# Kernel optimization log

Hardware: AMD Instinct MI355X
Metric: run time of the kernel (lower is better)

The kernel has to match this reference:

```python
import jax, jax.numpy as jnp
import numpy as np

B, S, H = 4, 2048, 768
ROUTING_GAIN = 1.0
LN_EPS = 1e-5
MAS_EPS = 1e-9


def _mas_normalize(logits):
    m = jnp.max(jnp.abs(logits), axis=-1, keepdims=True)
    return jax.nn.relu(logits / (m + MAS_EPS))


def _layer_norm(x, w, b):
    mu = jnp.mean(x, axis=-1, keepdims=True)
    var = jnp.var(x, axis=-1, keepdims=True)
    return (x - mu) / jnp.sqrt(var + LN_EPS) * w + b


def _spl(x, proto, gate, mu_w, mu_b):
    # SparseProtoLinear: comp = x @ mu_w.T + mu_b ; match = x @ proto.T / sqrt(d_in) ; gate_logit = x @ gate.T
    scale = 1.0 / jnp.sqrt(jnp.asarray(x.shape[-1], x.dtype))
    match = jnp.einsum('bsd,od->bso', x, proto) * scale
    gate_logit = jnp.einsum('bsd,od->bso', x, gate)
    comp = jnp.einsum('bsd,od->bso', x, mu_w) + mu_b
    return comp, match, gate_logit


def _gate_branch(inp, comp, match, gate_logit):
    routing_logits = (match - _mas_normalize(gate_logit)) * ROUTING_GAIN
    return (inp + comp) * _mas_normalize(routing_logits)


def _rotate_half(x):
    x1, x2 = jnp.split(x, 2, axis=-1)
    return jnp.concatenate([-x2, x1], axis=-1)


def _apply_rope(q, k, cos, sin):
    return q * cos + _rotate_half(q) * sin, k * cos + _rotate_half(k) * sin


def _causal_attention(q, k, v):
    # single-head SDPA over full hidden dim, causal
    d = q.shape[-1]
    scores = jnp.einsum('bqd,bkd->bqk', q, k) / jnp.sqrt(jnp.asarray(d, q.dtype))
    mask = jnp.tril(jnp.ones((q.shape[1], k.shape[1]), dtype=bool))
    scores = jnp.where(mask, scores, jnp.asarray(-jnp.inf, scores.dtype))
    p = jax.nn.softmax(scores, axis=-1)
    return jnp.einsum('bqk,bkd->bqd', p, v)


def setup_inputs() -> dict:
    key = jax.random.key(0)
    ks = iter(jax.random.split(key, 32))
    w_std = 1.0 / np.sqrt(H)
    inp = {'x': jax.random.normal(next(ks), (B, S, H), jnp.float32)}
    # rotary tables: half-dim frequencies duplicated to full hidden dim
    inv_freq = 1.0 / (10000.0 ** (np.arange(0, H, 2, dtype=np.float32) / H))
    ang = np.arange(S, dtype=np.float32)[:, None] * inv_freq[None, :]  # [S, H/2]
    ang = np.concatenate([ang, ang], axis=-1)  # [S, H]
    inp['cos'] = jnp.asarray(np.cos(ang))
    inp['sin'] = jnp.asarray(np.sin(ang))
    inp['ln1_w'] = jnp.ones((H,), jnp.float32)
    inp['ln1_b'] = jnp.zeros((H,), jnp.float32)
    inp['ln2_w'] = jnp.ones((H,), jnp.float32)
    inp['ln2_b'] = jnp.zeros((H,), jnp.float32)
    for name in ['q', 'k', 'v', 'o', 'f1', 'f2']:
        inp[f'{name}_proto'] = jax.random.normal(next(ks), (H, H), jnp.float32) * w_std
        inp[f'{name}_gate'] = jax.random.normal(next(ks), (H, H), jnp.float32) * w_std
        inp[f'{name}_mu_w'] = jax.random.normal(next(ks), (H, H), jnp.float32) * w_std
        inp[f'{name}_mu_b'] = jnp.zeros((H,), jnp.float32)
    return inp


def reference(x, cos, sin, ln1_w, ln1_b, ln2_w, ln2_b,
              q_proto, q_gate, q_mu_w, q_mu_b,
              k_proto, k_gate, k_mu_w, k_mu_b,
              v_proto, v_gate, v_mu_w, v_mu_b,
              o_proto, o_gate, o_mu_w, o_mu_b,
              f1_proto, f1_gate, f1_mu_w, f1_mu_b,
              f2_proto, f2_gate, f2_mu_w, f2_mu_b):
    # prev_protos is None => effective_proto == proto_weight; past_kv is None => causal attention
    ln1_out = _layer_norm(x, ln1_w, ln1_b)
    c_q, mv_q, pc_q = _spl(ln1_out, q_proto, q_gate, q_mu_w, q_mu_b)
    c_k, mv_k, pc_k = _spl(ln1_out, k_proto, k_gate, k_mu_w, k_mu_b)
    c_v, mv_v, pc_v = _spl(ln1_out, v_proto, v_gate, v_mu_w, v_mu_b)
    q = _gate_branch(ln1_out, c_q, mv_q, pc_q)
    k = _gate_branch(ln1_out, c_k, mv_k, pc_k)
    v = _gate_branch(ln1_out, c_v, mv_v, pc_v)
    q, k = _apply_rope(q, k, cos, sin)
    attn_out = _causal_attention(q, k, v)
    c_o, mv_o, pc_o = _spl(attn_out, o_proto, o_gate, o_mu_w, o_mu_b)
    m_o = _gate_branch(attn_out, c_o, mv_o, pc_o)
    x = x + m_o
    ln2_out = _layer_norm(x, ln2_w, ln2_b)
    c1, mv1, pc1 = _spl(ln2_out, f1_proto, f1_gate, f1_mu_w, f1_mu_b)
    h_act = jax.nn.relu(_gate_branch(ln2_out, c1, mv1, pc1))
    c2, mv2, pc2 = _spl(h_act, f2_proto, f2_gate, f2_mu_w, f2_mu_b)
    m2 = _gate_branch(h_act, c2, mv2, pc2)
    x_out = x + m2
    return x_out
```

## Files before the change

kernel.cpp:

```cpp
#include <hip/hip_runtime.h>
#include <hip/hip_bf16.h>
#include <math.h>

#define B_ 4
#define S_ 2048
#define H_ 768
#define M_ (B_*S_)
#define MN ((size_t)M_*(size_t)H_)
#define HH (H_*H_)
#define SS ((size_t)S_*(size_t)S_)
#define SH ((size_t)S_*(size_t)H_)
#define NQKV 6912
#define N3   2304

typedef __bf16 bf16_t;
typedef __bf16 bf16x8 __attribute__((ext_vector_type(8)));
typedef __bf16 bf16x4 __attribute__((ext_vector_type(4)));
typedef float  f32x4  __attribute__((ext_vector_type(4)));
typedef unsigned short u16;
typedef u16 u16x4 __attribute__((ext_vector_type(4)));
typedef u16 u16x8 __attribute__((ext_vector_type(8)));

typedef __attribute__((address_space(3))) void       lds_void_t;
typedef __attribute__((address_space(1))) const void gvoid_t;

__device__ __forceinline__ float b2f(u16 u){ unsigned x = (unsigned)u << 16; float f; __builtin_memcpy(&f,&x,4); return f; }
__device__ __forceinline__ u16 f2b(float f){ bf16_t h = (bf16_t)f; u16 u; __builtin_memcpy(&u,&h,2); return u; }

template<bool MAXOP>
__device__ __forceinline__ float blockReduce(float v, float* s){
  #pragma unroll
  for (int o = 32; o; o >>= 1){
    float t = __shfl_xor(v, o);
    v = MAXOP ? fmaxf(v, t) : (v + t);
  }
  int lane = threadIdx.x & 63, w = threadIdx.x >> 6;
  if (lane == 0) s[w] = v;
  __syncthreads();
  float r = s[0];
  #pragma unroll
  for (int i = 1; i < 4; i++) r = MAXOP ? fmaxf(r, s[i]) : (r + s[i]);
  __syncthreads();
  return r;
}

__device__ __forceinline__ float waveMax(float v){
  #pragma unroll
  for (int o = 1; o < 64; o <<= 1) v = fmaxf(v, __shfl_xor(v, o));
  return v;
}
__device__ __forceinline__ float waveSum(float v){
  #pragma unroll
  for (int o = 1; o < 64; o <<= 1) v += __shfl_xor(v, o);
  return v;
}

struct W18 { const float* p[18]; };

__global__ __launch_bounds__(256) void conv_weights(W18 w, bf16_t* __restrict__ out, float rs){
  int m = blockIdx.y;
  float sc = (m % 3 == 1) ? rs : 1.0f;
  int i = (blockIdx.x * 256 + threadIdx.x) * 4;
  f32x4 v = *(const f32x4*)(w.p[m] + i);
  bf16x4 o; o[0]=(bf16_t)(v[0]*sc); o[1]=(bf16_t)(v[1]*sc); o[2]=(bf16_t)(v[2]*sc); o[3]=(bf16_t)(v[3]*sc);
  *(bf16x4*)(out + (size_t)m * HH + i) = o;
}

__global__ __launch_bounds__(256) void ln_kernel(const float* __restrict__ x,
                                                 const float* __restrict__ w,
                                                 const float* __restrict__ b,
                                                 bf16_t* __restrict__ outb){
  int wid = threadIdx.x >> 6, l = threadIdx.x & 63;
  int row = blockIdx.x * 4 + wid;
  size_t base = (size_t)row * H_ + l*12;
  float v[12];
  #pragma unroll
  for (int i = 0; i < 3; i++){
    f32x4 t = *(const f32x4*)(x + base + 4*i);
    #pragma unroll
    for (int j = 0; j < 4; j++) v[4*i+j] = t[j];
  }
  float s1 = 0.f, s2 = 0.f;
  #pragma unroll
  for (int j = 0; j < 12; j++){ s1 += v[j]; s2 += v[j]*v[j]; }
  s1 = waveSum(s1); s2 = waveSum(s2);
  float mu = s1 * (1.f/H_), var = s2 * (1.f/H_) - mu*mu;
  float rstd = rsqrtf(var + 1e-5f);
  #pragma unroll
  for (int i = 0; i < 3; i++){
    f32x4 wv = *(const f32x4*)(w + l*12 + 4*i);
    f32x4 bv = *(const f32x4*)(b + l*12 + 4*i);
    u16x4 u;
    #pragma unroll
    for (int j = 0; j < 4; j++) u[j] = f2b((v[4*i+j]-mu)*rstd*wv[j] + bv[j]);
    *(u16x4*)(outb + base + 4*i) = u;
  }
}

__global__ __launch_bounds__(256, 5) void gemm_bt(const bf16_t* __restrict__ A,
                                                  const bf16_t* __restrict__ Bm,
                                                  bf16_t* __restrict__ C,
                                                  int M, int N, int K,
                                                  long sA, long sB, long sC, int cmode){
  __shared__ bf16_t As[2][128*32];
  __shared__ bf16_t Bs[2][128*32];

  int gx = gridDim.x, gy = gridDim.y;
  int nwg = gx * gy * gridDim.z;
  int id  = (blockIdx.z * gy + blockIdx.y) * gx + blockIdx.x;
  int cpx = nwg >> 3;
  int nrb = cpx / gx;
  int x   = id & 7;
  int local = id >> 3;
  int bx  = local / nrb;
  int frow = x * nrb + (local % nrb);
  int by  = frow % gy;
  int z   = frow / gy;

  A  += (size_t)z * sA;
  Bm += (size_t)z * sB;
  C  += (size_t)z * sC;

  int row0 = by * 128, col0 = bx * 128;
  if (cmode == 1 && col0 > row0) return;

  int tid  = threadIdx.x;
  int lane = tid & 63;
  int wave = tid >> 6;
  int wm = wave >> 1, wn = wave & 1;
  int lr = lane & 15, kg = lane >> 4;

  f32x4 acc[4][4] = {};
  int NT = K >> 5;
  if (cmode == 2) { int lim = (row0 + 128) >> 5; NT = NT < lim ? NT : lim; }

  auto stage = [&](int buf, int kt){
    int kk = kt * 32;
    #pragma unroll
    for (int i = 0; i < 2; i++){
      int c  = tid + i*256;
      int r  = c >> 2;
      int scol = ((c & 3) ^ ((r >> 1) & 3)) * 8;
      __builtin_amdgcn_global_load_lds((gvoid_t*)(A  + (size_t)(row0 + r)*K + kk + scol),
                                       (lds_void_t*)(&As[buf][c*8]), 16, 0, 0);
      __builtin_amdgcn_global_load_lds((gvoid_t*)(Bm + (size_t)(col0 + r)*K + kk + scol),
                                       (lds_void_t*)(&Bs[buf][c*8]), 16, 0, 0);
    }
  };

  stage(0, 0);
  asm volatile("s_waitcnt vmcnt(0)" ::: "memory");
  __builtin_amdgcn_s_barrier();

  int buf = 0;
  for (int kt = 0; kt < NT; ++kt){
    if (kt + 1 < NT) stage(buf ^ 1, kt + 1);
    bf16x8 af[4], bfr[4];
    #pragma unroll
    for (int m = 0; m < 4; m++){
      int r = wm*64 + m*16 + lr;
      af[m] = *reinterpret_cast<const bf16x8*>(&As[buf][r*32 + ((kg ^ ((r >> 1) & 3)) * 8)]);
    }
    #pragma unroll
    for (int n = 0; n < 4; n++){
      int r = wn*64 + n*16 + lr;
      bfr[n] = *reinterpret_cast<const bf16x8*>(&Bs[buf][r*32 + ((kg ^ ((r >> 1) & 3)) * 8)]);
    }
    #pragma unroll
    for (int m = 0; m < 4; m++)
      #pragma unroll
      for (int n = 0; n < 4; n++)
        acc[m][n] = __builtin_amdgcn_mfma_f32_16x16x32_bf16(af[m], bfr[n], acc[m][n], 0, 0, 0);
    if (kt + 1 < NT) asm volatile("s_waitcnt vmcnt(0)" ::: "memory");
    __builtin_amdgcn_s_barrier();
    buf ^= 1;
  }

  #pragma unroll
  for (int m = 0; m < 4; m++){
    int rb = row0 + wm*64 + m*16 + kg*4;
    #pragma unroll
    for (int n = 0; n < 4; n++){
      int cc = col0 + wn*64 + n*16 + lr;
      #pragma unroll
      for (int r = 0; r < 4; r++)
        C[(size_t)(rb + r)*N + cc] = (bf16_t)acc[m][n][r];
    }
  }
}

__global__ __launch_bounds__(256) void gate_qkv(const bf16_t* __restrict__ inp,
                                                const bf16_t* __restrict__ c3,
                                                const float* __restrict__ b_q,
                                                const float* __restrict__ b_k,
                                                const float* __restrict__ b_v,
                                                const float* __restrict__ cosT,
                                                const float* __restrict__ sinT,
                                                bf16_t* __restrict__ q_o,
                                                bf16_t* __restrict__ k_o,
                                                bf16_t* __restrict__ v_o,
                                                float rs){
  int wid = threadIdx.x >> 6, l = threadIdx.x & 63;
  int row = blockIdx.x * 4 + wid;
  size_t bi = (size_t)row * H_ + l*12;
  size_t brow = (size_t)row * NQKV + l*12;

  float iv[12];
  #pragma unroll
  for (int i = 0; i < 3; i++){
    u16x4 a = *(const u16x4*)(inp + bi + 4*i);
    #pragma unroll
    for (int j = 0; j < 4; j++) iv[4*i+j] = b2f(a[j]);
  }
  int s = row & (S_ - 1);
  f32x4 cw[3], sw[3];
  #pragma unroll
  for (int i = 0; i < 3; i++){
    cw[i] = *(const f32x4*)(cosT + (size_t)s*H_ + l*12 + 4*i);
    sw[i] = *(const f32x4*)(sinT + (size_t)s*H_ + l*12 + 4*i);
  }

  const float* biasp[3] = {b_q, b_k, b_v};
  bf16_t* outp[3] = {q_o, k_o, v_o};

  #pragma unroll
  for (int sec = 0; sec < 3; sec++){
    size_t bc = brow + (size_t)sec * 2304;
    float cv[12], mv[12], gv[12];
    float gmax = 0.f;
    #pragma unroll
    for (int i = 0; i < 3; i++){
      u16x4 b = *(const u16x4*)(c3 + bc + 4*i);
      u16x4 c = *(const u16x4*)(c3 + bc + 768 + 4*i);
      u16x4 d = *(const u16x4*)(c3 + bc + 1536 + 4*i);
      f32x4 bv = *(const f32x4*)(biasp[sec] + l*12 + 4*i);
      #pragma unroll
      for (int j = 0; j < 4; j++){
        cv[4*i+j] = b2f(b[j]) + bv[j];
        mv[4*i+j] = b2f(c[j]);
        gv[4*i+j] = b2f(d[j]);
        gmax = fmaxf(gmax, fabsf(gv[4*i+j]));
      }
    }
    gmax = waveMax(gmax);
    float rg = 1.f / (gmax + 1e-9f);
    float rt[12], rmax = 0.f;
    #pragma unroll
    for (int j = 0; j < 12; j++){
      rt[j] = mv[j] - fmaxf(gv[j]*rg, 0.f);
      rmax  = fmaxf(rmax, fabsf(rt[j]));
    }
    rmax = waveMax(rmax);
    float rr = 1.f / (rmax + 1e-9f);
    float oscale = (sec == 0) ? rs : 1.0f;
    float val[12];
    #pragma unroll
    for (int j = 0; j < 12; j++) val[j] = (iv[j] + cv[j]) * fmaxf(rt[j]*rr, 0.f) * oscale;

    if (sec < 2){
      #pragma unroll
      for (int i = 0; i < 3; i++){
        u16x4 u;
        #pragma unroll
        for (int j = 0; j < 4; j++){
          int q = 4*i + j;
          float partner = __shfl_xor(val[q], 32);
          if (l < 32) partner = -partner;
          u[j] = f2b(val[q]*cw[i][j] + partner*sw[i][j]);
        }
        *(u16x4*)(outp[sec] + bi + 4*i) = u;
      }
    } else {
      #pragma unroll
      for (int i = 0; i < 3; i++){
        u16x4 u;
        #pragma unroll
        for (int j = 0; j < 4; j++) u[j] = f2b(val[4*i+j]);
        *(u16x4*)(outp[sec] + bi + 4*i) = u;
      }
    }
  }
}

__global__ __launch_bounds__(256) void gate_kernel(const bf16_t* __restrict__ inp,
                                                   const bf16_t* __restrict__ c3,
                                                   long ldc, int colbase,
                                                   const float* __restrict__ bias,
                                                   const float* __restrict__ resid,
                                                   const float* __restrict__ lnw,
                                                   const float* __restrict__ lnb,
                                                   float* __restrict__ outf,
                                                   bf16_t* __restrict__ outb,
                                                   int mode){
  int wid = threadIdx.x >> 6, l = threadIdx.x & 63;
  int row = blockIdx.x * 4 + wid;
  size_t bi = (size_t)row * H_ + l*12;
  size_t bc = (size_t)row * ldc + colbase + l*12;

  float iv[12], cv[12], mv[12], gv[12];
  float gmax = 0.f;
  #pragma unroll
  for (int i = 0; i < 3; i++){
    u16x4 a = *(const u16x4*)(inp + bi + 4*i);
    u16x4 b = *(const u16x4*)(c3 + bc + 4*i);
    u16x4 c = *(const u16x4*)(c3 + bc + 768 + 4*i);
    u16x4 d = *(const u16x4*)(c3 + bc + 1536 + 4*i);
    f32x4 bv = *(const f32x4*)(bias + l*12 + 4*i);
    #pragma unroll
    for (int j = 0; j < 4; j++){
      iv[4*i+j] = b2f(a[j]); cv[4*i+j] = b2f(b[j]) + bv[j];
      mv[4*i+j] = b2f(c[j]); gv[4*i+j] = b2f(d[j]);
      gmax = fmaxf(gmax, fabsf(gv[4*i+j]));
    }
  }
  gmax = waveMax(gmax);
  float rg = 1.f / (gmax + 1e-9f);

  float rt[12], rmax = 0.f;
  #pragma unroll
  for (int j = 0; j < 12; j++){
    rt[j] = mv[j] - fmaxf(gv[j]*rg, 0.f);
    rmax  = fmaxf(rmax, fabsf(rt[j]));
  }
  rmax = waveMax(rmax);
  float rr = 1.f / (rmax + 1e-9f);

  float val[12];
  #pragma unroll
  for (int j = 0; j < 12; j++) val[j] = (iv[j] + cv[j]) * fmaxf(rt[j]*rr, 0.f);

  if (mode == 3){
    #pragma unroll
    for (int i = 0; i < 3; i++){
      u16x4 u;
      #pragma unroll
      for (int j = 0; j < 4; j++) u[j] = f2b(fmaxf(val[4*i+j], 0.f));
      *(u16x4*)(outb + bi + 4*i) = u;
    }
  } else if (mode == 2){
    #pragma unroll
    for (int i = 0; i < 3; i++){
      f32x4 rv = *(const f32x4*)(resid + bi + 4*i);
      f32x4 ov;
      #pragma unroll
      for (int j = 0; j < 4; j++) ov[j] = val[4*i+j] + rv[j];
      *(f32x4*)(outf + bi + 4*i) = ov;
    }
  } else {
    float xv[12];
    #pragma unroll
    for (int i = 0; i < 3; i++){
      f32x4 rv = *(const f32x4*)(resid + bi + 4*i);
      f32x4 ov;
      #pragma unroll
      for (int j = 0; j < 4; j++){ xv[4*i+j] = val[4*i+j] + rv[j]; ov[j] = xv[4*i+j]; }
      *(f32x4*)(outf + bi + 4*i) = ov;
    }
    float s1 = 0.f, s2 = 0.f;
    #pragma unroll
    for (int j = 0; j < 12; j++){ s1 += xv[j]; s2 += xv[j]*xv[j]; }
    s1 = waveSum(s1); s2 = waveSum(s2);
    float mu = s1 * (1.f/H_), var = s2 * (1.f/H_) - mu*mu;
    float rstd = rsqrtf(var + 1e-5f);
    #pragma unroll
    for (int i = 0; i < 3; i++){
      f32x4 wv = *(const f32x4*)(lnw + l*12 + 4*i);
      f32x4 bv = *(const f32x4*)(lnb + l*12 + 4*i);
      u16x4 u;
      #pragma unroll
      for (int j = 0; j < 4; j++) u[j] = f2b((xv[4*i+j]-mu)*rstd*wv[j] + bv[j]);
      *(u16x4*)(outb + bi + 4*i) = u;
    }
  }
}

__global__ __launch_bounds__(256) void softmax_causal(const bf16_t* __restrict__ sc,
                                                      bf16_t* __restrict__ P){
  __shared__ float red[4];
  int r = blockIdx.x, b = blockIdx.y, t = threadIdx.x;
  const bf16_t* srow = sc + (size_t)b*SS + (size_t)r * S_;
  bf16_t* prow = P + (size_t)b*SS + (size_t)r * S_;
  int n = r + 1;
  int fill = ((r >> 7) + 1) << 7;
  int c0 = t * 8;

  float v[8];
  float m = -1e30f;
  if (c0 < n){
    u16x8 u = *(const u16x8*)(srow + c0);
    #pragma unroll
    for (int j = 0; j < 8; j++){
      v[j] = (c0 + j < n) ? b2f(u[j]) : -1e30f;
      m = fmaxf(m, v[j]);
    }
  } else {
    #pragma unroll
    for (int j = 0; j < 8; j++) v[j] = -1e30f;
  }
  m = blockReduce<true>(m, red);
  float sum = 0.f;
  #pragma unroll
  for (int j = 0; j < 8; j++){
    v[j] = (v[j] > -1e29f) ? __expf(v[j] - m) : 0.f;
    sum += v[j];
  }
  sum = blockReduce<false>(sum, red);
  float inv = 1.f / sum;
  if (c0 < fill){
    u16x8 u;
    #pragma unroll
    for (int j = 0; j < 8; j++) u[j] = f2b(v[j] * inv);
    *(u16x8*)(prow + c0) = u;
  }
}

__global__ __launch_bounds__(256) void transpose_bf(const bf16_t* __restrict__ in,
                                                    bf16_t* __restrict__ out){
  __shared__ bf16_t tile[32][33];
  int bz = blockIdx.z;
  const bf16_t* I = in  + (size_t)bz * SH;
  bf16_t*       O = out + (size_t)bz * SH;
  int s0 = blockIdx.x*32, h0 = blockIdx.y*32;
  int tx = threadIdx.x, ty = threadIdx.y;
  #pragma unroll
  for (int k = 0; k < 4; k++)
    tile[ty + 8*k][tx] = I[(size_t)(s0 + ty + 8*k)*H_ + h0 + tx];
  __syncthreads();
  #pragma unroll
  for (int k = 0; k < 4; k++)
    O[(size_t)(h0 + ty + 8*k)*S_ + s0 + tx] = tile[tx][ty + 8*k];
}

extern "C" void kernel_launch(void* const* d_in, const int* in_sizes, int n_in,
                              void* d_out, int out_size, void* d_ws, size_t ws_size,
                              hipStream_t stream){
  const float* x    = (const float*)d_in[0];
  const float* cosT = (const float*)d_in[1];
  const float* sinT = (const float*)d_in[2];
  const float* ln1w = (const float*)d_in[3];
  const float* ln1b = (const float*)d_in[4];
  const float* ln2w = (const float*)d_in[5];
  const float* ln2b = (const float*)d_in[6];

  W18 wp; const float* bias[6];
  for (int i = 0; i < 6; i++){
    const float* proto = (const float*)d_in[7 + 4*i + 0];
    const float* gatep = (const float*)d_in[7 + 4*i + 1];
    const float* muw   = (const float*)d_in[7 + 4*i + 2];
    bias[i]            = (const float*)d_in[7 + 4*i + 3];
    wp.p[i*3 + 0] = muw;
    wp.p[i*3 + 1] = proto;
    wp.p[i*3 + 2] = gatep;
  }

  char* w = (char*)d_ws;
  auto alloc = [&](size_t bytes){ void* r = (void*)w; w += (bytes + 255) & ~(size_t)255; return r; };
  bf16_t* w_bf   = (bf16_t*)alloc((size_t)18 * HH * 2);
  bf16_t* a_bf   = (bf16_t*)alloc(MN * 2);
  bf16_t* h_bf   = (bf16_t*)alloc(MN * 2);
  bf16_t* c3b    = (bf16_t*)alloc((size_t)M_ * NQKV * 2);
  bf16_t* q_bf   = (bf16_t*)alloc(MN * 2);
  bf16_t* k_bf   = (bf16_t*)alloc(MN * 2);
  bf16_t* v_bf   = (bf16_t*)alloc(MN * 2);
  bf16_t* vt     = (bf16_t*)alloc(MN * 2);
  bf16_t* attn_b = (bf16_t*)alloc(MN * 2);
  float*  x1     = (float*) alloc(MN * 4);
  (void)ws_size;
  bf16_t* sc_bf = c3b;
  bf16_t* p_bf  = c3b + B_ * SS;

  const float rs = 1.0f / sqrtf((float)H_);

  conv_weights<<<dim3(HH/1024, 18), 256, 0, stream>>>(wp, w_bf, rs);
  ln_kernel<<<M_/4, 256, 0, stream>>>(x, ln1w, ln1b, a_bf);

  gemm_bt<<<dim3(NQKV/128, M_/128, 1), 256, 0, stream>>>(
      a_bf, w_bf, c3b, M_, NQKV, H_, 0, 0, 0, 0);
  gate_qkv<<<M_/4, 256, 0, stream>>>(a_bf, c3b, bias[0], bias[1], bias[2],
                                     cosT, sinT, q_bf, k_bf, v_bf, rs);

  transpose_bf<<<dim3(S_/32, H_/32, B_), dim3(32, 8), 0, stream>>>(v_bf, vt);

  gemm_bt<<<dim3(S_/128, S_/128, B_), 256, 0, stream>>>(
      q_bf, k_bf, sc_bf, S_, S_, H_, (long)SH, (long)SH, (long)SS, 1);

  softmax_causal<<<dim3(S_, B_), 256, 0, stream>>>(sc_bf, p_bf);

  gemm_bt<<<dim3(H_/128, S_/128, B_), 256, 0, stream>>>(
      p_bf, vt, attn_b, S_, H_, S_, (long)SS, (long)SH, (long)SH, 2);

  gemm_bt<<<dim3(N3/128, M_/128, 1), 256, 0, stream>>>(
      attn_b, w_bf + (size_t)9*HH, c3b, M_, N3, H_, 0, 0, 0, 0);
  gate_kernel<<<M_/4, 256, 0, stream>>>(attn_b, c3b, N3, 0, bias[3], x, ln2w, ln2b, x1, a_bf, 4);

  gemm_bt<<<dim3(N3/128, M_/128, 1), 256, 0, stream>>>(
      a_bf, w_bf + (size_t)12*HH, c3b, M_, N3, H_, 0, 0, 0, 0);
  gate_kernel<<<M_/4, 256, 0, stream>>>(a_bf, c3b, N3, 0, bias[4], nullptr, nullptr, nullptr, nullptr, h_bf, 3);

  gemm_bt<<<dim3(N3/128, M_/128, 1), 256, 0, stream>>>(
      h_bf, w_bf + (size_t)15*HH, c3b, M_, N3, H_, 0, 0, 0, 0);
  gate_kernel<<<M_/4, 256, 0, stream>>>(h_bf, c3b, N3, 0, bias[5], x1, nullptr, nullptr, (float*)d_out, nullptr, 2);
}
```

Measured before the change: 494.3 us.

## Add 256x256 phased GEMM kernel for QKV and causal score GEMMs

Introduces a 512-thread GEMM with 256x256 tiles, 64-wide K steps, 128KB dynamic LDS, and a four-phase schedule that interleaves LDS reads, async global-to-LDS loads and MFMA quads using setprio and barriers. The QKV projection and the causal QK^T score GEMM now use it, the latter with a compact triangular tile enumeration so no blocks are launched above the diagonal. The remaining 128x128 GEMM moves from double to triple buffering, prefetching two stages ahead. Bigger tiles cut global traffic per FLOP and the deeper pipeline hides load latency, at the cost of lower occupancy and more LDS per block.

New measurement: 431.3 us. -12.8%, faster.

```diff
diff --git a/kernel.cpp b/kernel.cpp
--- a/kernel.cpp
+++ b/kernel.cpp
@@ -97,13 +97,160 @@
   }
 }
 
-__global__ __launch_bounds__(256, 5) void gemm_bt(const bf16_t* __restrict__ A,
-                                                  const bf16_t* __restrict__ Bm,
-                                                  bf16_t* __restrict__ C,
-                                                  int M, int N, int K,
-                                                  long sA, long sB, long sC, int cmode){
-  __shared__ bf16_t As[2][128*32];
-  __shared__ bf16_t Bs[2][128*32];
+template<int MB, int NB>
+__device__ __forceinline__ void quad(f32x4 (&acc)[8][4], bf16x8 (&aF)[8][2], bf16x8 (&bF)[4][2]){
+  #pragma unroll
+  for (int m = MB; m < MB+4; m++)
+    #pragma unroll
+    for (int n = NB; n < NB+2; n++){
+      acc[m][n] = __builtin_amdgcn_mfma_f32_16x16x32_bf16(aF[m][0], bF[n][0], acc[m][n], 0,0,0);
+      acc[m][n] = __builtin_amdgcn_mfma_f32_16x16x32_bf16(aF[m][1], bF[n][1], acc[m][n], 0,0,0);
+    }
+}
+
+__global__ __launch_bounds__(512, 2) void gemm256ph(const bf16_t* __restrict__ A,
+                                                    const bf16_t* __restrict__ Bm,
+                                                    bf16_t* __restrict__ C,
+                                                    int M, int N, int K,
+                                                    long sA, long sB, long sC, int causal){
+  extern __shared__ char smem[];
+  char* Ab = smem;
+  char* Bb = smem + 65536;
+
+  int bx, by, z;
+  if (causal){
+    int id = blockIdx.x;
+    z = id / 36; int t = id % 36;
+    by = 0;
+    while ((by+1)*(by+2)/2 <= t) by++;
+    bx = t - by*(by+1)/2;
+  } else {
+    int gx = gridDim.x, gy = gridDim.y;
+    int nwg = gx * gy;
+    int id  = blockIdx.y * gx + blockIdx.x;
+    int cpx = nwg >> 3;
+    int nrb = cpx / gx;
+    int x = id & 7; int local = id >> 3;
+    bx = local / nrb;
+    by = x * nrb + (local % nrb);
+    z = 0;
+  }
+
+  A  += (size_t)z * sA;
+  Bm += (size_t)z * sB;
+  C  += (size_t)z * sC;
+  int row0 = by * 256, col0 = bx * 256;
+
+  int tid = threadIdx.x, lane = tid & 63, wid = tid >> 6;
+  int wm = wid >> 2, wn = wid & 3;
+  int lr = lane & 15, kg = lane >> 4;
+  int NT = K >> 6;
+
+  auto stA = [&](int buf, int h, int kt){
+    #pragma unroll
+    for (int i = 0; i < 2; i++){
+      int cc = tid + i*512;
+      int rl = cc >> 3, sl = cc & 7;
+      const bf16_t* src = A + (size_t)(row0 + h*128 + rl)*K + kt*64 + (sl ^ (rl & 7))*8;
+      char* dst = Ab + buf*32768 + h*16384 + cc*16;
+      __builtin_amdgcn_global_load_lds((gvoid_t*)src, (lds_void_t*)dst, 16, 0, 0);
+    }
+  };
+  auto stB = [&](int buf, int h, int kt){
+    #pragma unroll
+    for (int i = 0; i < 2; i++){
+      int cc = tid + i*512;
+      int rl = cc >> 3, sl = cc & 7;
+      const bf16_t* src = Bm + (size_t)(col0 + h*128 + rl)*K + kt*64 + (sl ^ (rl & 7))*8;
+      char* dst = Bb + buf*32768 + h*16384 + cc*16;
+      __builtin_amdgcn_global_load_lds((gvoid_t*)src, (lds_void_t*)dst, 16, 0, 0);
+    }
+  };
+  auto rd = [&](char* base, int buf, int r, int kh) -> bf16x8 {
+    return *(const bf16x8*)(base + buf*32768 + r*128 + (((kh<<2)+kg) ^ (r & 7))*16);
+  };
+
+  f32x4 acc[8][4] = {};
+  bf16x8 aF[8][2], bF[4][2];
+
+  stA(0,0,0); stA(0,1,0); stB(0,0,0); stB(0,1,0);
+  if (NT > 1){ stB(1,0,1); stB(1,1,1);
+    asm volatile("s_waitcnt vmcnt(4)" ::: "memory");
+  } else {
+    asm volatile("s_waitcnt vmcnt(0)" ::: "memory");
+  }
+  __builtin_amdgcn_s_barrier();
+
+  int buf = 0;
+  for (int t = 0; t < NT; ++t){
+    int nb = buf ^ 1;
+    #pragma unroll
+    for (int m = 0; m < 4; m++){ int r = wm*128 + m*16 + lr;
+      aF[m][0] = rd(Ab, buf, r, 0); aF[m][1] = rd(Ab, buf, r, 1); }
+    #pragma unroll
+    for (int n = 0; n < 2; n++){ int r = wn*64 + n*16 + lr;
+      bF[n][0] = rd(Bb, buf, r, 0); bF[n][1] = rd(Bb, buf, r, 1); }
+    if (t + 1 < NT) stA(nb, 0, t+1);
+    __builtin_amdgcn_s_barrier();
+    asm volatile("s_waitcnt lgkmcnt(0)" ::: "memory");
+    __builtin_amdgcn_sched_barrier(0);
+    __builtin_amdgcn_s_setprio(1);
+    quad<0,0>(acc, aF, bF);
+    __builtin_amdgcn_s_setprio(0);
+    __builtin_amdgcn_s_barrier();
+    #pragma unroll
+    for (int n = 2; n < 4; n++){ int r = wn*64 + n*16 + lr;
+      bF[n][0] = rd(Bb, buf, r, 0); bF[n][1] = rd(Bb, buf, r, 1); }
+    if (t + 1 < NT) stA(nb, 1, t+1);
+    __builtin_amdgcn_s_barrier();
+    asm volatile("s_waitcnt lgkmcnt(0)" ::: "memory");
+    __builtin_amdgcn_sched_barrier(0);
+    __builtin_amdgcn_s_setprio(1);
+    quad<0,2>(acc, aF, bF);
+    __builtin_amdgcn_s_setprio(0);
+    __builtin_amdgcn_s_barrier();
+    #pragma unroll
+    for (int m = 4; m < 8; m++){ int r = wm*128 + m*16 + lr;
+      aF[m][0] = rd(Ab, buf, r, 0); aF[m][1] = rd(Ab, buf, r, 1); }
+    if (t + 2 < NT) stB(buf, 0, t+2);
+    __builtin_amdgcn_s_barrier();
+    asm volatile("s_waitcnt lgkmcnt(0)" ::: "memory");
+    __builtin_amdgcn_sched_barrier(0);
+    __builtin_amdgcn_s_setprio(1);
+    quad<4,0>(acc, aF, bF);
+    __builtin_amdgcn_s_setprio(0);
+    __builtin_amdgcn_s_barrier();
+    if (t + 2 < NT) stB(buf, 1, t+2);
+    __builtin_amdgcn_s_barrier();
+    __builtin_amdgcn_s_setprio(1);
+    quad<4,2>(acc, aF, bF);
+    __builtin_amdgcn_s_setprio(0);
+    if (t + 2 < NT)      asm volatile("s_waitcnt vmcnt(4)" ::: "memory");
+    else if (t + 1 < NT) asm volatile("s_waitcnt vmcnt(0)" ::: "memory");
+    __builtin_amdgcn_s_barrier();
+    buf = nb;
+  }
+
+  #pragma unroll
+  for (int m = 0; m < 8; m++){
+    int rb = row0 + wm*128 + m*16 + kg*4;
+    #pragma unroll
+    for (int n = 0; n < 4; n++){
+      int cc = col0 + wn*64 + n*16 + lr;
+      #pragma unroll
+      for (int r = 0; r < 4; r++)
+        C[(size_t)(rb + r)*N + cc] = (bf16_t)acc[m][n][r];
+    }
+  }
+}
+
+__global__ __launch_bounds__(256) void gemm_bt(const bf16_t* __restrict__ A,
+                                               const bf16_t* __restrict__ Bm,
+                                               bf16_t* __restrict__ C,
+                                               int M, int N, int K,
+                                               long sA, long sB, long sC, int cmode){
+  __shared__ bf16_t As[3][128*32];
+  __shared__ bf16_t Bs[3][128*32];
 
   int gx = gridDim.x, gy = gridDim.y;
   int nwg = gx * gy * gridDim.z;
@@ -122,7 +269,6 @@
   C  += (size_t)z * sC;
 
   int row0 = by * 128, col0 = bx * 128;
-  if (cmode == 1 && col0 > row0) return;
 
   int tid  = threadIdx.x;
   int lane = tid & 63;
@@ -149,31 +295,37 @@
   };
 
   stage(0, 0);
-  asm volatile("s_waitcnt vmcnt(0)" ::: "memory");
+  stage(1, 1);
+  asm volatile("s_waitcnt vmcnt(4)" ::: "memory");
   __builtin_amdgcn_s_barrier();
-
-  int buf = 0;
+  __builtin_amdgcn_sched_barrier(0);
+
+  int b0 = 0, b1 = 1, b2 = 2;
   for (int kt = 0; kt < NT; ++kt){
-    if (kt + 1 < NT) stage(buf ^ 1, kt + 1);
+    if (kt + 2 < NT) stage(b2, kt + 2);
     bf16x8 af[4], bfr[4];
     #pragma unroll
     for (int m = 0; m < 4; m++){
       int r = wm*64 + m*16 + lr;
-      af[m] = *reinterpret_cast<const bf16x8*>(&As[buf][r*32 + ((kg ^ ((r >> 1) & 3)) * 8)]);
+      af[m] = *reinterpret_cast<const bf16x8*>(&As[b0][r*32 + ((kg ^ ((r >> 1) & 3)) * 8)]);
     }
     #pragma unroll
     for (int n = 0; n < 4; n++){
       int r = wn*64 + n*16 + lr;
-      bfr[n] = *reinterpret_cast<const bf16x8*>(&Bs[buf][r*32 + ((kg ^ ((r >> 1) & 3)) * 8)]);
+      bfr[n] = *reinterpret_cast<const bf16x8*>(&Bs[b0][r*32 + ((kg ^ ((r >> 1) & 3)) * 8)]);
     }
     #pragma unroll
     for (int m = 0; m < 4; m++)
       #pragma unroll
       for (int n = 0; n < 4; n++)
         acc[m][n] = __builtin_amdgcn_mfma_f32_16x16x32_bf16(af[m], bfr[n], acc[m][n], 0, 0, 0);
-    if (kt + 1 < NT) asm volatile("s_waitcnt vmcnt(0)" ::: "memory");
-    __builtin_amdgcn_s_barrier();
-    buf ^= 1;
+    if (kt + 1 < NT){
+      if (kt + 2 < NT) asm volatile("s_waitcnt vmcnt(4)" ::: "memory");
+      else             asm volatile("s_waitcnt vmcnt(0)" ::: "memory");
+      __builtin_amdgcn_s_barrier();
+      __builtin_amdgcn_sched_barrier(0);
+    }
+    int tmp = b0; b0 = b1; b1 = b2; b2 = tmp;
   }
 
   #pragma unroll
@@ -453,6 +605,8 @@
     wp.p[i*3 + 2] = gatep;
   }
 
+  hipFuncSetAttribute((const void*)gemm256ph, hipFuncAttributeMaxDynamicSharedMemorySize, 131072);
+
   char* w = (char*)d_ws;
   auto alloc = [&](size_t bytes){ void* r = (void*)w; w += (bytes + 255) & ~(size_t)255; return r; };
   bf16_t* w_bf   = (bf16_t*)alloc((size_t)18 * HH * 2);
@@ -474,14 +628,14 @@
   conv_weights<<<dim3(HH/1024, 18), 256, 0, stream>>>(wp, w_bf, rs);
   ln_kernel<<<M_/4, 256, 0, stream>>>(x, ln1w, ln1b, a_bf);
 
-  gemm_bt<<<dim3(NQKV/128, M_/128, 1), 256, 0, stream>>>(
+  gemm256ph<<<dim3(NQKV/256, M_/256, 1), 512, 131072, stream>>>(
       a_bf, w_bf, c3b, M_, NQKV, H_, 0, 0, 0, 0);
   gate_qkv<<<M_/4, 256, 0, stream>>>(a_bf, c3b, bias[0], bias[1], bias[2],
                                      cosT, sinT, q_bf, k_bf, v_bf, rs);
 
   transpose_bf<<<dim3(S_/32, H_/32, B_), dim3(32, 8), 0, stream>>>(v_bf, vt);
 
-  gemm_bt<<<dim3(S_/128, S_/128, B_), 256, 0, stream>>>(
+  gemm256ph<<<dim3(36*B_, 1, 1), 512, 131072, stream>>>(
       q_bf, k_bf, sc_bf, S_, S_, H_, (long)SH, (long)SH, (long)SS, 1);
 
   softmax_causal<<<dim3(S_, B_), 256, 0, stream>>>(sc_bf, p_bf);
```
